# Optimization experiments

Hardware: AMD Instinct MI355X
Metric: run time of the kernel (lower is better)

Reference implementation:

```python
import jax, jax.numpy as jnp
import numpy as np

B, LQ, LK = 2, 4096, 512
Q_DIM, KV_DIM, D_ATTN, N_HEADS = 1024, 1024, 1024, 16
HDIM = D_ATTN // N_HEADS
LOOKBACK = 4
ROPE_MAX = 8192


def rope_tables(smax, hdim):
    inv_freq = 1.0 / (10000.0 ** (jnp.arange(0, hdim, 2, dtype=jnp.float32) / hdim))
    freqs = jnp.arange(smax, dtype=jnp.float32)[:, None] * inv_freq[None, :]  # [S, hdim/2]
    emb = jnp.concatenate([freqs, freqs], axis=-1)  # [S, hdim]
    return jnp.cos(emb), jnp.sin(emb)


def rotate_half(x):
    h = x.shape[-1] // 2
    return jnp.concatenate([-x[..., h:], x[..., :h]], axis=-1)


def setup_inputs() -> dict:
    key = jax.random.key(0)
    ks = jax.random.split(key, 8)
    q = jax.random.normal(ks[0], (B, LQ, Q_DIM), dtype=jnp.float32)
    kv = jax.random.normal(ks[1], (B, LK, KV_DIM), dtype=jnp.float32)
    q_pos_ids = jax.random.randint(ks[2], (B, LQ), 0, 4096)
    kv_pos_ids = jax.random.randint(ks[3], (LK,), 0, 4096)
    seg_id = jnp.sort(jax.random.randint(ks[4], (B, LQ), 0, LK), axis=-1)
    sc = 1.0 / np.sqrt(Q_DIM)
    Wq = jax.random.normal(ks[5], (Q_DIM, D_ATTN), dtype=jnp.float32) * sc
    Wkv = jax.random.normal(ks[6], (KV_DIM, 2 * D_ATTN), dtype=jnp.float32) * sc
    Wo = jax.random.normal(ks[7], (D_ATTN, Q_DIM), dtype=jnp.float32) * sc
    return {"q": q, "kv": kv, "q_pos_ids": q_pos_ids, "kv_pos_ids": kv_pos_ids,
            "seg_id": seg_id, "Wq": Wq, "Wkv": Wkv, "Wo": Wo}


def reference(q, kv, q_pos_ids, kv_pos_ids, seg_id, Wq, Wkv, Wo):
    Bq, Lq, _ = q.shape
    Lk = kv.shape[1]
    # projections + split heads -> [B, H, L, hdim]
    qh = (q @ Wq).reshape(Bq, Lq, N_HEADS, HDIM).transpose(0, 2, 1, 3)
    kvl = kv @ Wkv
    kh = kvl[..., :D_ATTN].reshape(Bq, Lk, N_HEADS, HDIM).transpose(0, 2, 1, 3)
    vh = kvl[..., D_ATTN:].reshape(Bq, Lk, N_HEADS, HDIM).transpose(0, 2, 1, 3)
    # gathered RoPE
    cos, sin = rope_tables(ROPE_MAX, HDIM)  # [S, hdim]
    qp = jnp.clip(q_pos_ids, 0, ROPE_MAX - 1)
    q_cos = cos[qp][:, None]  # [B,1,Lq,hdim]
    q_sin = sin[qp][:, None]
    qh = qh * q_cos + rotate_half(qh) * q_sin
    kp = jnp.clip(kv_pos_ids, 0, ROPE_MAX - 1)
    k_cos = cos[kp][None, None]  # [1,1,Lk,hdim]
    k_sin = sin[kp][None, None]
    kh = kh * k_cos + rotate_half(kh) * k_sin
    # segment lookback mask: keep iff seg_id - lookback <= k <= seg_id
    kidx = jnp.arange(Lk)
    keep = (kidx[None, None, :] <= seg_id[:, :, None]) & \
           (kidx[None, None, :] >= seg_id[:, :, None] - LOOKBACK)  # [B,Lq,Lk]
    scale = 1.0 / np.sqrt(HDIM)
    scores = jnp.einsum('bhqd,bhkd->bhqk', qh, kh) * scale
    scores = jnp.where(keep[:, None], scores, -jnp.inf)
    attn = jax.nn.softmax(scores, axis=-1)
    ctx = jnp.einsum('bhqk,bhkd->bhqd', attn, vh)
    out = ctx.transpose(0, 2, 1, 3).reshape(Bq, Lq, D_ATTN)
    return out @ Wo
```

## Files before the change

### kernel.cpp

```cpp
#include <hip/hip_runtime.h>
#include <math.h>


typedef unsigned short u16;
typedef __attribute__((ext_vector_type(8))) short bhalf8;
typedef __attribute__((ext_vector_type(4))) float fvec4;

__device__ __forceinline__ u16 f2bf(float f) {
  unsigned u = __float_as_uint(f);
  u += 0x7fffu + ((u >> 16) & 1u);
  return (u16)(u >> 16);
}
__device__ __forceinline__ float bf2f(u16 h) {
  return __uint_as_float(((unsigned)h) << 16);
}

__global__ __launch_bounds__(256) void prep_kernel(
    const float* __restrict__ Wq, const float* __restrict__ Wkv,
    const float* __restrict__ Wo, u16* __restrict__ WqT,
    u16* __restrict__ WkvT, u16* __restrict__ WoT,
    const float* __restrict__ q, u16* __restrict__ qb,
    const float* __restrict__ kv, u16* __restrict__ kvb,
    float2* __restrict__ csT) {
  const int bid = blockIdx.x;
  if (bid < 4096) {
    __shared__ float tile[32][33];
    const float* W;
    u16* Wt;
    int N, t;
    if (bid < 1024)      { W = Wq;  Wt = WqT;  N = 1024; t = bid; }
    else if (bid < 3072) { W = Wkv; Wt = WkvT; N = 2048; t = bid - 1024; }
    else                 { W = Wo;  Wt = WoT;  N = 1024; t = bid - 3072; }
    const int sh = (N >> 11) + 5;
    const int n0 = (t & ((1 << sh) - 1)) << 5;
    const int k0 = (t >> sh) << 5;
    const int tx = threadIdx.x & 31, ty = threadIdx.x >> 5;
#pragma unroll
    for (int i = 0; i < 32; i += 8)
      tile[ty + i][tx] = W[(size_t)(k0 + ty + i) * N + n0 + tx];
    __syncthreads();
#pragma unroll
    for (int i = 0; i < 32; i += 8)
      Wt[(size_t)(n0 + ty + i) * 1024 + k0 + tx] = f2bf(tile[tx][ty + i]);
    return;
  }
  const int NQ4 = 2097152, NKV4 = 262144, NR = 131072;
  const int stride = 2048 * 256;
  for (int u = (bid - 4096) * 256 + threadIdx.x; u < NQ4 + NKV4 + NR; u += stride) {
    if (u < NQ4) {
      const float4 v = ((const float4*)q)[u];
      ushort4 o;
      o.x = f2bf(v.x); o.y = f2bf(v.y); o.z = f2bf(v.z); o.w = f2bf(v.w);
      ((ushort4*)qb)[u] = o;
    } else if (u < NQ4 + NKV4) {
      const int i = u - NQ4;
      const float4 v = ((const float4*)kv)[i];
      ushort4 o;
      o.x = f2bf(v.x); o.y = f2bf(v.y); o.z = f2bf(v.z); o.w = f2bf(v.w);
      ((ushort4*)kvb)[i] = o;
    } else {
      const int i = u - NQ4 - NKV4;
      const int pos = i >> 5, j = i & 31;
      const float invf = expf(-(float)j * 0.28782313662425572f);
      float s, c;
      sincosf((float)pos * invf, &s, &c);
      csT[i] = make_float2(c, s);
    }
  }
}

__device__ __forceinline__ void gemm_core_128_db(
    const u16* __restrict__ A, const u16* __restrict__ Bt,
    int m0, int n0, fvec4 acc[4][4], u16* As, u16* Bs) {
  const int tid = threadIdx.x;
  const int lane = tid & 63;
  const int wv = tid >> 6, wm = wv >> 1, wn = wv & 1;

  int a_off[4], b_off[4];
#pragma unroll
  for (int i = 0; i < 4; ++i) {
    const int rA = wm * 64 + i * 16 + (lane & 15);
    a_off[i] = rA * 32 + (((lane >> 4) ^ ((rA >> 1) & 3)) << 3);
    const int rB = wn * 64 + i * 16 + (lane & 15);
    b_off[i] = rB * 32 + (((lane >> 4) ^ ((rB >> 1) & 3)) << 3);
  }
  const int i0 = tid, i1 = tid + 256;
  const int r0 = i0 >> 2, g0 = (i0 & 3) ^ ((r0 >> 1) & 3);
  const int r1 = i1 >> 2, g1 = (i1 & 3) ^ ((r1 >> 1) & 3);
  const u16* a0 = A + (size_t)(m0 + r0) * 1024 + g0 * 8;
  const u16* a1 = A + (size_t)(m0 + r1) * 1024 + g1 * 8;
  const u16* b0 = Bt + (size_t)(n0 + r0) * 1024 + g0 * 8;
  const u16* b1 = Bt + (size_t)(n0 + r1) * 1024 + g1 * 8;

#define STAGE_DB(buf, kk)                                                    \
  do {                                                                       \
    u16* As_ = As + (buf) * 4096;                                            \
    u16* Bs_ = Bs + (buf) * 4096;                                            \
    __builtin_amdgcn_global_load_lds(                                        \
        (__attribute__((address_space(1))) void*)(a0 + (kk)),                \
        (__attribute__((address_space(3))) void*)(As_ + i0 * 8), 16, 0, 0);  \
    __builtin_amdgcn_global_load_lds(                                        \
        (__attribute__((address_space(1))) void*)(a1 + (kk)),                \
        (__attribute__((address_space(3))) void*)(As_ + i1 * 8), 16, 0, 0);  \
    __builtin_amdgcn_global_load_lds(                                        \
        (__attribute__((address_space(1))) void*)(b0 + (kk)),                \
        (__attribute__((address_space(3))) void*)(Bs_ + i0 * 8), 16, 0, 0);  \
    __builtin_amdgcn_global_load_lds(                                        \
        (__attribute__((address_space(1))) void*)(b1 + (kk)),                \
        (__attribute__((address_space(3))) void*)(Bs_ + i1 * 8), 16, 0, 0);  \
  } while (0)

  STAGE_DB(0, 0);
  STAGE_DB(1, 32);
  asm volatile("s_waitcnt vmcnt(4)" ::: "memory");
  __builtin_amdgcn_s_barrier();

#pragma unroll
  for (int t = 0; t < 32; ++t) {
    const int cur = t % 3;
    const int nx2 = (t + 2) % 3;
    const int k2 = t * 32 + 64;
    if (k2 < 1024) STAGE_DB(nx2, k2);
    const int co = cur * 4096;
    bhalf8 af[4], bfv[4];
#pragma unroll
    for (int i = 0; i < 4; ++i) af[i] = *(const bhalf8*)(As + co + a_off[i]);
#pragma unroll
    for (int i = 0; i < 4; ++i) bfv[i] = *(const bhalf8*)(Bs + co + b_off[i]);
    __builtin_amdgcn_s_setprio(1);
#pragma unroll
    for (int mi = 0; mi < 4; ++mi)
#pragma unroll
      for (int ni = 0; ni < 4; ++ni)
        acc[mi][ni] = __builtin_amdgcn_mfma_f32_16x16x32_bf16(
            af[mi], bfv[ni], acc[mi][ni], 0, 0, 0);
    __builtin_amdgcn_s_setprio(0);
    if (k2 < 1024) {
      asm volatile("s_waitcnt vmcnt(4)" ::: "memory");
    } else {
      asm volatile("s_waitcnt vmcnt(0)" ::: "memory");
    }
    __builtin_amdgcn_s_barrier();
  }
#undef STAGE_DB
}

#define GEMM_PROLOGUE()                                              \
  __shared__ __align__(16) u16 As[3 * 128 * 32];                     \
  __shared__ __align__(16) u16 Bs[3 * 128 * 32];                     \
  fvec4 acc[4][4];                                                   \
  _Pragma("unroll") for (int i = 0; i < 4; ++i)                      \
      _Pragma("unroll") for (int j = 0; j < 4; ++j)                  \
          acc[i][j] = (fvec4){0.f, 0.f, 0.f, 0.f};

__global__ __launch_bounds__(256) void gemm12_kernel(
    const u16* __restrict__ qA, const u16* __restrict__ WqT,
    const u16* __restrict__ kvA, const u16* __restrict__ WkvT,
    u16* __restrict__ qh, u16* __restrict__ kh, u16* __restrict__ vh,
    const int* __restrict__ qpos, const int* __restrict__ kpos,
    const float2* __restrict__ csT) {
  GEMM_PROLOGUE();
  const int swz = ((blockIdx.x & 7) * 80) + (blockIdx.x >> 3);
  const int lane = threadIdx.x & 63;
  const int wv = threadIdx.x >> 6, wm = wv >> 1, wn = wv & 1;

  if (swz < 512) {
    const int m0 = (swz >> 3) * 128, n0 = (swz & 7) * 128;
    gemm_core_128_db(qA, WqT, m0, n0, acc, As, Bs);
#pragma unroll
    for (int mi = 0; mi < 4; ++mi) {
#pragma unroll
      for (int r = 0; r < 4; ++r) {
        const int rowg = m0 + wm * 64 + mi * 16 + (lane >> 4) * 4 + r;
        int pos = qpos[rowg];
        pos = pos < 0 ? 0 : (pos > 4095 ? 4095 : pos);
#pragma unroll
        for (int ni = 0; ni < 2; ++ni) {
          const int j = ni * 16 + (lane & 15);
          const float2 cs = csT[pos * 32 + j];
          const float x1 = acc[mi][ni][r], x2 = acc[mi][ni + 2][r];
          const int colg = n0 + wn * 64 + ni * 16 + (lane & 15);
          qh[(size_t)rowg * 1024 + colg]      = f2bf((x1 * cs.x - x2 * cs.y) * 0.125f);
          qh[(size_t)rowg * 1024 + colg + 32] = f2bf((x2 * cs.x + x1 * cs.y) * 0.125f);
        }
      }
    }
  } else {
    const int t = swz - 512;
    const int m0 = (t >> 4) * 128, n0 = (t & 15) * 128;
    gemm_core_128_db(kvA, WkvT, m0, n0, acc, As, Bs);
    const bool isK = (n0 + wn * 64) < 1024;
#pragma unroll
    for (int mi = 0; mi < 4; ++mi) {
#pragma unroll
      for (int r = 0; r < 4; ++r) {
        const int rowg = m0 + wm * 64 + mi * 16 + (lane >> 4) * 4 + r;
        if (isK) {
          int pos = kpos[rowg & 511];
          pos = pos < 0 ? 0 : (pos > 4095 ? 4095 : pos);
#pragma unroll
          for (int ni = 0; ni < 2; ++ni) {
            const int j = ni * 16 + (lane & 15);
            const float2 cs = csT[pos * 32 + j];
            const float x1 = acc[mi][ni][r], x2 = acc[mi][ni + 2][r];
            const int colg = n0 + wn * 64 + ni * 16 + (lane & 15);
            kh[(size_t)rowg * 1024 + colg]      = f2bf(x1 * cs.x - x2 * cs.y);
            kh[(size_t)rowg * 1024 + colg + 32] = f2bf(x2 * cs.x + x1 * cs.y);
          }
        } else {
#pragma unroll
          for (int ni = 0; ni < 4; ++ni) {
            const int colg = n0 + wn * 64 + ni * 16 + (lane & 15);
            vh[(size_t)rowg * 1024 + colg - 1024] = f2bf(acc[mi][ni][r]);
          }
        }
      }
    }
  }
}

__global__ __launch_bounds__(256) void gemm_out_kernel(
    const u16* __restrict__ A, const u16* __restrict__ Bt,
    float* __restrict__ out) {
  GEMM_PROLOGUE();
  const int wg = ((blockIdx.x & 7) << 6) + (blockIdx.x >> 3);
  const int m0 = (wg >> 3) * 128, n0 = (wg & 7) * 128;
  gemm_core_128_db(A, Bt, m0, n0, acc, As, Bs);
  const int lane = threadIdx.x & 63;
  const int wv = threadIdx.x >> 6, wm = wv >> 1, wn = wv & 1;
#pragma unroll
  for (int mi = 0; mi < 4; ++mi) {
#pragma unroll
    for (int r = 0; r < 4; ++r) {
      const int rowg = m0 + wm * 64 + mi * 16 + (lane >> 4) * 4 + r;
#pragma unroll
      for (int ni = 0; ni < 4; ++ni) {
        const int colg = n0 + wn * 64 + ni * 16 + (lane & 15);
        out[(size_t)rowg * 1024 + colg] = acc[mi][ni][r];
      }
    }
  }
}

__global__ __launch_bounds__(256) void attn_kernel(
    const u16* __restrict__ qh, const u16* __restrict__ kh,
    const u16* __restrict__ vh, const int* __restrict__ seg_id,
    u16* __restrict__ ctx) {
  const int lane = threadIdx.x & 63;
  const int row = (blockIdx.x * 256 + threadIdx.x) >> 6;
  const int b = row >> 12;
  const int sg = seg_id[row];
  const int kmin = sg > 4 ? sg - 4 : 0;

  const u16* qp = qh + (size_t)row * 1024 + lane * 16;
  const bhalf8 qa = *(const bhalf8*)qp;
  const bhalf8 qb = *(const bhalf8*)(qp + 8);
  float qv[16];
#pragma unroll
  for (int e = 0; e < 8; ++e) {
    qv[e] = bf2f((u16)qa[e]);
    qv[8 + e] = bf2f((u16)qb[e]);
  }

  float sc[5];
  float mx = -3.0e38f;
#pragma unroll
  for (int t = 0; t < 5; ++t) {
    const int k = kmin + t;
    const u16* kp = kh + (size_t)((b << 9) + k) * 1024 + lane * 16;
    const bhalf8 ka = *(const bhalf8*)kp;
    const bhalf8 kb = *(const bhalf8*)(kp + 8);
    float d = 0.f;
#pragma unroll
    for (int e = 0; e < 8; ++e)
      d += qv[e] * bf2f((u16)ka[e]) + qv[8 + e] * bf2f((u16)kb[e]);
    d += __shfl_xor(d, 1);
    d += __shfl_xor(d, 2);
    sc[t] = (k <= sg) ? d : -3.0e38f;
    mx = fmaxf(mx, sc[t]);
  }

  float den = 0.f;
  float o[16];
#pragma unroll
  for (int e = 0; e < 16; ++e) o[e] = 0.f;
#pragma unroll
  for (int t = 0; t < 5; ++t) {
    const float p = __expf(sc[t] - mx);
    den += p;
    const int k = kmin + t;
    const u16* vp = vh + (size_t)((b << 9) + k) * 1024 + lane * 16;
    const bhalf8 va = *(const bhalf8*)vp;
    const bhalf8 vb = *(const bhalf8*)(vp + 8);
#pragma unroll
    for (int e = 0; e < 8; ++e) {
      o[e] += p * bf2f((u16)va[e]);
      o[8 + e] += p * bf2f((u16)vb[e]);
    }
  }
  const float inv = 1.f / den;
  bhalf8 oa, ob;
#pragma unroll
  for (int e = 0; e < 8; ++e) {
    oa[e] = (short)f2bf(o[e] * inv);
    ob[e] = (short)f2bf(o[8 + e] * inv);
  }
  u16* cp = ctx + (size_t)row * 1024 + lane * 16;
  *(bhalf8*)cp = oa;
  *(bhalf8*)(cp + 8) = ob;
}

extern "C" void kernel_launch(void* const* d_in, const int* in_sizes, int n_in,
                              void* d_out, int out_size, void* d_ws, size_t ws_size,
                              hipStream_t stream) {
  const float* q   = (const float*)d_in[0];
  const float* kv  = (const float*)d_in[1];
  const int* qpos  = (const int*)d_in[2];
  const int* kpos  = (const int*)d_in[3];
  const int* seg   = (const int*)d_in[4];
  const float* Wq  = (const float*)d_in[5];
  const float* Wkv = (const float*)d_in[6];
  const float* Wo  = (const float*)d_in[7];
  float* out = (float*)d_out;

  char* w = (char*)d_ws;
  u16* qb    = (u16*)w; w += (size_t)8192 * 1024 * 2;
  u16* kvb   = (u16*)w; w += (size_t)1024 * 1024 * 2;
  u16* WqT   = (u16*)w; w += (size_t)1024 * 1024 * 2;
  u16* WkvT  = (u16*)w; w += (size_t)2048 * 1024 * 2;
  u16* WoT   = (u16*)w; w += (size_t)1024 * 1024 * 2;
  u16* qhB   = (u16*)w; w += (size_t)8192 * 1024 * 2;
  u16* khB   = (u16*)w; w += (size_t)1024 * 1024 * 2;
  u16* vhB   = (u16*)w; w += (size_t)1024 * 1024 * 2;
  u16* ctxB  = (u16*)w; w += (size_t)8192 * 1024 * 2;
  float2* csT = (float2*)w; w += (size_t)4096 * 32 * 8;

  prep_kernel<<<6144, 256, 0, stream>>>(Wq, Wkv, Wo, WqT, WkvT, WoT,
                                        q, qb, kv, kvb, csT);
  gemm12_kernel<<<640, 256, 0, stream>>>(qb, WqT, kvb, WkvT,
                                         qhB, khB, vhB, qpos, kpos, csT);
  attn_kernel<<<2048, 256, 0, stream>>>(qhB, khB, vhB, seg, ctxB);
  gemm_out_kernel<<<512, 256, 0, stream>>>(ctxB, WoT, out);
}
```

Measured before the change: 92.44 us.

## Split GEMM workgroups into producer and consumer waves for LDS staging

GEMM kernels now launch 512 threads: four waves issue global-to-LDS loads into a triple buffer, and four waves only read LDS and run MFMAs, synchronized by raw s_barrier. This is meant to keep the MFMA waves free of load issue and vmcnt waits. The trade-off is doubled workgroup size, which may reduce occupancy given the accumulator register footprint, plus idle producer waves during the epilogue.

```diff
diff --git a/kernel.cpp b/kernel.cpp
--- a/kernel.cpp
+++ b/kernel.cpp
@@ -69,30 +69,23 @@
   }
 }
 
-__device__ __forceinline__ void gemm_core_128_db(
+__device__ __forceinline__ void gemm_core_128_pc(
     const u16* __restrict__ A, const u16* __restrict__ Bt,
     int m0, int n0, fvec4 acc[4][4], u16* As, u16* Bs) {
   const int tid = threadIdx.x;
-  const int lane = tid & 63;
-  const int wv = tid >> 6, wm = wv >> 1, wn = wv & 1;
-
-  int a_off[4], b_off[4];
-#pragma unroll
-  for (int i = 0; i < 4; ++i) {
-    const int rA = wm * 64 + i * 16 + (lane & 15);
-    a_off[i] = rA * 32 + (((lane >> 4) ^ ((rA >> 1) & 3)) << 3);
-    const int rB = wn * 64 + i * 16 + (lane & 15);
-    b_off[i] = rB * 32 + (((lane >> 4) ^ ((rB >> 1) & 3)) << 3);
-  }
-  const int i0 = tid, i1 = tid + 256;
-  const int r0 = i0 >> 2, g0 = (i0 & 3) ^ ((r0 >> 1) & 3);
-  const int r1 = i1 >> 2, g1 = (i1 & 3) ^ ((r1 >> 1) & 3);
-  const u16* a0 = A + (size_t)(m0 + r0) * 1024 + g0 * 8;
-  const u16* a1 = A + (size_t)(m0 + r1) * 1024 + g1 * 8;
-  const u16* b0 = Bt + (size_t)(n0 + r0) * 1024 + g0 * 8;
-  const u16* b1 = Bt + (size_t)(n0 + r1) * 1024 + g1 * 8;
-
-#define STAGE_DB(buf, kk)                                                    \
+  const int wv = tid >> 6;
+
+  if (wv >= 4) {
+    const int t2 = tid & 255;
+    const int i0 = t2, i1 = t2 + 256;
+    const int r0 = i0 >> 2, g0 = (i0 & 3) ^ ((r0 >> 1) & 3);
+    const int r1 = i1 >> 2, g1 = (i1 & 3) ^ ((r1 >> 1) & 3);
+    const u16* a0 = A + (size_t)(m0 + r0) * 1024 + g0 * 8;
+    const u16* a1 = A + (size_t)(m0 + r1) * 1024 + g1 * 8;
+    const u16* b0 = Bt + (size_t)(n0 + r0) * 1024 + g0 * 8;
+    const u16* b1 = Bt + (size_t)(n0 + r1) * 1024 + g1 * 8;
+
+#define STAGE_PC(buf, kk)                                                    \
   do {                                                                       \
     u16* As_ = As + (buf) * 4096;                                            \
     u16* Bs_ = Bs + (buf) * 4096;                                            \
@@ -110,39 +103,52 @@
         (__attribute__((address_space(3))) void*)(Bs_ + i1 * 8), 16, 0, 0);  \
   } while (0)
 
-  STAGE_DB(0, 0);
-  STAGE_DB(1, 32);
-  asm volatile("s_waitcnt vmcnt(4)" ::: "memory");
-  __builtin_amdgcn_s_barrier();
-
-#pragma unroll
-  for (int t = 0; t < 32; ++t) {
-    const int cur = t % 3;
-    const int nx2 = (t + 2) % 3;
-    const int k2 = t * 32 + 64;
-    if (k2 < 1024) STAGE_DB(nx2, k2);
-    const int co = cur * 4096;
-    bhalf8 af[4], bfv[4];
-#pragma unroll
-    for (int i = 0; i < 4; ++i) af[i] = *(const bhalf8*)(As + co + a_off[i]);
-#pragma unroll
-    for (int i = 0; i < 4; ++i) bfv[i] = *(const bhalf8*)(Bs + co + b_off[i]);
-    __builtin_amdgcn_s_setprio(1);
-#pragma unroll
-    for (int mi = 0; mi < 4; ++mi)
-#pragma unroll
-      for (int ni = 0; ni < 4; ++ni)
-        acc[mi][ni] = __builtin_amdgcn_mfma_f32_16x16x32_bf16(
-            af[mi], bfv[ni], acc[mi][ni], 0, 0, 0);
-    __builtin_amdgcn_s_setprio(0);
-    if (k2 < 1024) {
-      asm volatile("s_waitcnt vmcnt(4)" ::: "memory");
-    } else {
-      asm volatile("s_waitcnt vmcnt(0)" ::: "memory");
-    }
-    __builtin_amdgcn_s_barrier();
-  }
-#undef STAGE_DB
+    STAGE_PC(0, 0);
+    STAGE_PC(1, 32);
+    asm volatile("s_waitcnt vmcnt(4)" ::: "memory");
+    asm volatile("s_barrier" ::: "memory");
+#pragma unroll
+    for (int t = 0; t < 32; ++t) {
+      if (t < 30) {
+        STAGE_PC((t + 2) % 3, (t + 2) * 32);
+        asm volatile("s_waitcnt vmcnt(4)" ::: "memory");
+      } else {
+        asm volatile("s_waitcnt vmcnt(0)" ::: "memory");
+      }
+      asm volatile("s_barrier" ::: "memory");
+    }
+#undef STAGE_PC
+  } else {
+    const int lane = tid & 63;
+    const int wm = wv >> 1, wn = wv & 1;
+    int a_off[4], b_off[4];
+#pragma unroll
+    for (int i = 0; i < 4; ++i) {
+      const int rA = wm * 64 + i * 16 + (lane & 15);
+      a_off[i] = rA * 32 + (((lane >> 4) ^ ((rA >> 1) & 3)) << 3);
+      const int rB = wn * 64 + i * 16 + (lane & 15);
+      b_off[i] = rB * 32 + (((lane >> 4) ^ ((rB >> 1) & 3)) << 3);
+    }
+    asm volatile("s_barrier" ::: "memory");
+#pragma unroll
+    for (int t = 0; t < 32; ++t) {
+      const int co = (t % 3) * 4096;
+      bhalf8 af[4], bfv[4];
+#pragma unroll
+      for (int i = 0; i < 4; ++i) af[i] = *(const bhalf8*)(As + co + a_off[i]);
+#pragma unroll
+      for (int i = 0; i < 4; ++i) bfv[i] = *(const bhalf8*)(Bs + co + b_off[i]);
+      __builtin_amdgcn_s_setprio(1);
+#pragma unroll
+      for (int mi = 0; mi < 4; ++mi)
+#pragma unroll
+        for (int ni = 0; ni < 4; ++ni)
+          acc[mi][ni] = __builtin_amdgcn_mfma_f32_16x16x32_bf16(
+              af[mi], bfv[ni], acc[mi][ni], 0, 0, 0);
+      __builtin_amdgcn_s_setprio(0);
+      asm volatile("s_barrier" ::: "memory");
+    }
+  }
 }
 
 #define GEMM_PROLOGUE()                                              \
@@ -153,7 +159,7 @@
       _Pragma("unroll") for (int j = 0; j < 4; ++j)                  \
           acc[i][j] = (fvec4){0.f, 0.f, 0.f, 0.f};
 
-__global__ __launch_bounds__(256) void gemm12_kernel(
+__global__ __launch_bounds__(512) void gemm12_kernel(
     const u16* __restrict__ qA, const u16* __restrict__ WqT,
     const u16* __restrict__ kvA, const u16* __restrict__ WkvT,
     u16* __restrict__ qh, u16* __restrict__ kh, u16* __restrict__ vh,
@@ -162,11 +168,23 @@
   GEMM_PROLOGUE();
   const int swz = ((blockIdx.x & 7) * 80) + (blockIdx.x >> 3);
   const int lane = threadIdx.x & 63;
-  const int wv = threadIdx.x >> 6, wm = wv >> 1, wn = wv & 1;
-
+  const int wv = threadIdx.x >> 6;
+  const int wm = (wv & 3) >> 1, wn = wv & 1;
+
+  const u16 *A, *Bt;
+  int m0, n0;
   if (swz < 512) {
-    const int m0 = (swz >> 3) * 128, n0 = (swz & 7) * 128;
-    gemm_core_128_db(qA, WqT, m0, n0, acc, As, Bs);
+    A = qA; Bt = WqT;
+    m0 = (swz >> 3) * 128; n0 = (swz & 7) * 128;
+  } else {
+    const int t = swz - 512;
+    A = kvA; Bt = WkvT;
+    m0 = (t >> 4) * 128; n0 = (t & 15) * 128;
+  }
+  gemm_core_128_pc(A, Bt, m0, n0, acc, As, Bs);
+  if (wv >= 4) return;
+
+  if (swz < 512) {
 #pragma unroll
     for (int mi = 0; mi < 4; ++mi) {
 #pragma unroll
@@ -186,9 +204,6 @@
       }
     }
   } else {
-    const int t = swz - 512;
-    const int m0 = (t >> 4) * 128, n0 = (t & 15) * 128;
-    gemm_core_128_db(kvA, WkvT, m0, n0, acc, As, Bs);
     const bool isK = (n0 + wn * 64) < 1024;
 #pragma unroll
     for (int mi = 0; mi < 4; ++mi) {
@@ -219,15 +234,17 @@
   }
 }
 
-__global__ __launch_bounds__(256) void gemm_out_kernel(
+__global__ __launch_bounds__(512) void gemm_out_kernel(
     const u16* __restrict__ A, const u16* __restrict__ Bt,
     float* __restrict__ out) {
   GEMM_PROLOGUE();
   const int wg = ((blockIdx.x & 7) << 6) + (blockIdx.x >> 3);
   const int m0 = (wg >> 3) * 128, n0 = (wg & 7) * 128;
-  gemm_core_128_db(A, Bt, m0, n0, acc, As, Bs);
+  gemm_core_128_pc(A, Bt, m0, n0, acc, As, Bs);
+  const int wv = threadIdx.x >> 6;
+  if (wv >= 4) return;
   const int lane = threadIdx.x & 63;
-  const int wv = threadIdx.x >> 6, wm = wv >> 1, wn = wv & 1;
+  const int wm = wv >> 1, wn = wv & 1;
 #pragma unroll
   for (int mi = 0; mi < 4; ++mi) {
 #pragma unroll
@@ -337,8 +354,8 @@
 
   prep_kernel<<<6144, 256, 0, stream>>>(Wq, Wkv, Wo, WqT, WkvT, WoT,
                                         q, qb, kv, kvb, csT);
-  gemm12_kernel<<<640, 256, 0, stream>>>(qb, WqT, kvb, WkvT,
+  gemm12_kernel<<<640, 512, 0, stream>>>(qb, WqT, kvb, WkvT,
                                          qhB, khB, vhB, qpos, kpos, csT);
   attn_kernel<<<2048, 256, 0, stream>>>(qhB, khB, vhB, seg, ctxB);
-  gemm_out_kernel<<<512, 256, 0, stream>>>(ctxB, WoT, out);
-}
+  gemm_out_kernel<<<512, 512, 0, stream>>>(ctxB, WoT, out);
+}
```

After: 93.00 us. No clear change (+0.6%).

## Switch GEMMs to 256x128 tiles with 512 threads and 8-phase pipelined K loop

Applied to the files above, without the earlier changes.

The GEMM core moves from 128x128 tiles with K-step 32 and 256 threads to 256x128 tiles with K-step 64 and 8 waves. The K loop is split into eight phases that interleave staged global-to-LDS loads with MFMA sub-blocks, using barriers between phases and a new XOR swizzle over 8 chunks. The aim is more reuse per loaded byte and better overlap of loads with MFMA. In exchange it uses much more LDS per block, launches half as many blocks (320 and 256), and adds barrier overhead.

```diff
diff --git a/kernel.cpp b/kernel.cpp
--- a/kernel.cpp
+++ b/kernel.cpp
@@ -5,6 +5,8 @@
 typedef unsigned short u16;
 typedef __attribute__((ext_vector_type(8))) short bhalf8;
 typedef __attribute__((ext_vector_type(4))) float fvec4;
+
+#define MFMA(a, b, c) __builtin_amdgcn_mfma_f32_16x16x32_bf16((a), (b), (c), 0, 0, 0)
 
 __device__ __forceinline__ u16 f2bf(float f) {
   unsigned u = __float_as_uint(f);
@@ -69,104 +71,150 @@
   }
 }
 
-__device__ __forceinline__ void gemm_core_128_db(
+__device__ __forceinline__ void gemm_core_8ph(
     const u16* __restrict__ A, const u16* __restrict__ Bt,
     int m0, int n0, fvec4 acc[4][4], u16* As, u16* Bs) {
   const int tid = threadIdx.x;
   const int lane = tid & 63;
   const int wv = tid >> 6, wm = wv >> 1, wn = wv & 1;
 
-  int a_off[4], b_off[4];
-#pragma unroll
-  for (int i = 0; i < 4; ++i) {
-    const int rA = wm * 64 + i * 16 + (lane & 15);
-    a_off[i] = rA * 32 + (((lane >> 4) ^ ((rA >> 1) & 3)) << 3);
-    const int rB = wn * 64 + i * 16 + (lane & 15);
-    b_off[i] = rB * 32 + (((lane >> 4) ^ ((rB >> 1) & 3)) << 3);
-  }
-  const int i0 = tid, i1 = tid + 256;
-  const int r0 = i0 >> 2, g0 = (i0 & 3) ^ ((r0 >> 1) & 3);
-  const int r1 = i1 >> 2, g1 = (i1 & 3) ^ ((r1 >> 1) & 3);
-  const u16* a0 = A + (size_t)(m0 + r0) * 1024 + g0 * 8;
-  const u16* a1 = A + (size_t)(m0 + r1) * 1024 + g1 * 8;
-  const u16* b0 = Bt + (size_t)(n0 + r0) * 1024 + g0 * 8;
-  const u16* b1 = Bt + (size_t)(n0 + r1) * 1024 + g1 * 8;
-
-#define STAGE_DB(buf, kk)                                                    \
+  const u16* aglb[4];
+  int aldst[4];
+#pragma unroll
+  for (int j = 0; j < 4; ++j) {
+    const int cidx = tid + j * 512;
+    const int row = cidx >> 3, g = (cidx & 7) ^ (row & 7);
+    aglb[j] = A + (size_t)(m0 + row) * 1024 + g * 8;
+    aldst[j] = cidx * 8;
+  }
+  const u16* bglb[2];
+  int bldst[2];
+#pragma unroll
+  for (int j = 0; j < 2; ++j) {
+    const int cidx = tid + j * 512;
+    const int row = cidx >> 3, g = (cidx & 7) ^ (row & 7);
+    bglb[j] = Bt + (size_t)(n0 + row) * 1024 + g * 8;
+    bldst[j] = cidx * 8;
+  }
+
+#define LD_A(buf, kk, j)                                                     \
+  __builtin_amdgcn_global_load_lds(                                          \
+      (__attribute__((address_space(1))) void*)(aglb[j] + (kk)),             \
+      (__attribute__((address_space(3))) void*)(As + (buf) * 16384 + aldst[j]), 16, 0, 0)
+#define LD_B(buf, kk, j)                                                     \
+  __builtin_amdgcn_global_load_lds(                                          \
+      (__attribute__((address_space(1))) void*)(bglb[j] + (kk)),             \
+      (__attribute__((address_space(3))) void*)(Bs + (buf) * 8192 + bldst[j]), 16, 0, 0)
+
+  const int c = lane >> 4;
+  const int sl0 = ((c) ^ (lane & 7)) * 8;
+  const int sl1 = ((c + 4) ^ (lane & 7)) * 8;
+  const int rba = (wm * 64 + (lane & 15)) * 64;
+  const int rbb = (wn * 64 + (lane & 15)) * 64;
+
+#define PH(bufi, QM, QN, STAGE, TAIL)                                        \
   do {                                                                       \
-    u16* As_ = As + (buf) * 4096;                                            \
-    u16* Bs_ = Bs + (buf) * 4096;                                            \
-    __builtin_amdgcn_global_load_lds(                                        \
-        (__attribute__((address_space(1))) void*)(a0 + (kk)),                \
-        (__attribute__((address_space(3))) void*)(As_ + i0 * 8), 16, 0, 0);  \
-    __builtin_amdgcn_global_load_lds(                                        \
-        (__attribute__((address_space(1))) void*)(a1 + (kk)),                \
-        (__attribute__((address_space(3))) void*)(As_ + i1 * 8), 16, 0, 0);  \
-    __builtin_amdgcn_global_load_lds(                                        \
-        (__attribute__((address_space(1))) void*)(b0 + (kk)),                \
-        (__attribute__((address_space(3))) void*)(Bs_ + i0 * 8), 16, 0, 0);  \
-    __builtin_amdgcn_global_load_lds(                                        \
-        (__attribute__((address_space(1))) void*)(b1 + (kk)),                \
-        (__attribute__((address_space(3))) void*)(Bs_ + i1 * 8), 16, 0, 0);  \
+    STAGE;                                                                   \
+    const u16* Ab = As + (bufi) * 16384 + rba;                               \
+    const u16* Bb = Bs + (bufi) * 8192 + rbb;                                \
+    const bhalf8 a00 = *(const bhalf8*)(Ab + (QM * 2) * 1024 + sl0);         \
+    const bhalf8 a01 = *(const bhalf8*)(Ab + (QM * 2) * 1024 + sl1);         \
+    const bhalf8 a10 = *(const bhalf8*)(Ab + (QM * 2 + 1) * 1024 + sl0);     \
+    const bhalf8 a11 = *(const bhalf8*)(Ab + (QM * 2 + 1) * 1024 + sl1);     \
+    const bhalf8 b00 = *(const bhalf8*)(Bb + (QN * 2) * 1024 + sl0);         \
+    const bhalf8 b01 = *(const bhalf8*)(Bb + (QN * 2) * 1024 + sl1);         \
+    const bhalf8 b10 = *(const bhalf8*)(Bb + (QN * 2 + 1) * 1024 + sl0);     \
+    const bhalf8 b11 = *(const bhalf8*)(Bb + (QN * 2 + 1) * 1024 + sl1);     \
+    __builtin_amdgcn_s_barrier();                                            \
+    __builtin_amdgcn_s_setprio(1);                                           \
+    acc[QM * 2][QN * 2]         = MFMA(a00, b00, acc[QM * 2][QN * 2]);       \
+    acc[QM * 2][QN * 2]         = MFMA(a01, b01, acc[QM * 2][QN * 2]);       \
+    acc[QM * 2][QN * 2 + 1]     = MFMA(a00, b10, acc[QM * 2][QN * 2 + 1]);   \
+    acc[QM * 2][QN * 2 + 1]     = MFMA(a01, b11, acc[QM * 2][QN * 2 + 1]);   \
+    acc[QM * 2 + 1][QN * 2]     = MFMA(a10, b00, acc[QM * 2 + 1][QN * 2]);   \
+    acc[QM * 2 + 1][QN * 2]     = MFMA(a11, b01, acc[QM * 2 + 1][QN * 2]);   \
+    acc[QM * 2 + 1][QN * 2 + 1] = MFMA(a10, b10, acc[QM * 2 + 1][QN * 2 + 1]);\
+    acc[QM * 2 + 1][QN * 2 + 1] = MFMA(a11, b11, acc[QM * 2 + 1][QN * 2 + 1]);\
+    __builtin_amdgcn_s_setprio(0);                                           \
+    TAIL;                                                                    \
   } while (0)
 
-  STAGE_DB(0, 0);
-  STAGE_DB(1, 32);
-  asm volatile("s_waitcnt vmcnt(4)" ::: "memory");
+#define BAR __builtin_amdgcn_s_barrier()
+#define VMTAIL(st)                                                           \
+  do {                                                                       \
+    if (st) asm volatile("s_waitcnt vmcnt(6)" ::: "memory");                 \
+    else    asm volatile("s_waitcnt vmcnt(0)" ::: "memory");                 \
+    __builtin_amdgcn_s_barrier();                                            \
+  } while (0)
+
+#pragma unroll
+  for (int j = 0; j < 4; ++j) LD_A(0, 0, j);
+#pragma unroll
+  for (int j = 0; j < 2; ++j) LD_B(0, 0, j);
+#pragma unroll
+  for (int j = 0; j < 4; ++j) LD_A(1, 64, j);
+#pragma unroll
+  for (int j = 0; j < 2; ++j) LD_B(1, 64, j);
+  asm volatile("s_waitcnt vmcnt(6)" ::: "memory");
   __builtin_amdgcn_s_barrier();
 
-#pragma unroll
-  for (int t = 0; t < 32; ++t) {
-    const int cur = t % 3;
-    const int nx2 = (t + 2) % 3;
-    const int k2 = t * 32 + 64;
-    if (k2 < 1024) STAGE_DB(nx2, k2);
-    const int co = cur * 4096;
-    bhalf8 af[4], bfv[4];
-#pragma unroll
-    for (int i = 0; i < 4; ++i) af[i] = *(const bhalf8*)(As + co + a_off[i]);
-#pragma unroll
-    for (int i = 0; i < 4; ++i) bfv[i] = *(const bhalf8*)(Bs + co + b_off[i]);
-    __builtin_amdgcn_s_setprio(1);
-#pragma unroll
-    for (int mi = 0; mi < 4; ++mi)
-#pragma unroll
-      for (int ni = 0; ni < 4; ++ni)
-        acc[mi][ni] = __builtin_amdgcn_mfma_f32_16x16x32_bf16(
-            af[mi], bfv[ni], acc[mi][ni], 0, 0, 0);
-    __builtin_amdgcn_s_setprio(0);
-    if (k2 < 1024) {
-      asm volatile("s_waitcnt vmcnt(4)" ::: "memory");
-    } else {
-      asm volatile("s_waitcnt vmcnt(0)" ::: "memory");
-    }
-    __builtin_amdgcn_s_barrier();
-  }
-#undef STAGE_DB
+  int b0 = 0;
+#pragma unroll 1
+  for (int it = 0; it < 8; ++it) {
+    const int b1 = (b0 == 2) ? 0 : b0 + 1;
+    const int b2 = (b1 == 2) ? 0 : b1 + 1;
+    const int kk2 = it * 128 + 128;
+    const int kk3 = it * 128 + 192;
+    const bool st = it < 7;
+    PH(b0, 0, 0, if (st) { LD_A(b2, kk2, 0); LD_A(b2, kk2, 1); }, BAR);
+    PH(b0, 0, 1, if (st) { LD_A(b2, kk2, 2); LD_A(b2, kk2, 3); }, BAR);
+    PH(b0, 1, 0, if (st) { LD_B(b2, kk2, 0); LD_B(b2, kk2, 1); }, BAR);
+    PH(b0, 1, 1, (void)0, VMTAIL(st));
+    PH(b1, 0, 0, if (st) { LD_A(b0, kk3, 0); LD_A(b0, kk3, 1); }, BAR);
+    PH(b1, 0, 1, if (st) { LD_A(b0, kk3, 2); LD_A(b0, kk3, 3); }, BAR);
+    PH(b1, 1, 0, if (st) { LD_B(b0, kk3, 0); LD_B(b0, kk3, 1); }, BAR);
+    PH(b1, 1, 1, (void)0, VMTAIL(st));
+    b0 = b2;
+  }
+#undef PH
+#undef BAR
+#undef VMTAIL
+#undef LD_A
+#undef LD_B
 }
 
 #define GEMM_PROLOGUE()                                              \
-  __shared__ __align__(16) u16 As[3 * 128 * 32];                     \
-  __shared__ __align__(16) u16 Bs[3 * 128 * 32];                     \
+  __shared__ __align__(16) u16 As[3 * 256 * 64];                     \
+  __shared__ __align__(16) u16 Bs[3 * 128 * 64];                     \
   fvec4 acc[4][4];                                                   \
   _Pragma("unroll") for (int i = 0; i < 4; ++i)                      \
       _Pragma("unroll") for (int j = 0; j < 4; ++j)                  \
           acc[i][j] = (fvec4){0.f, 0.f, 0.f, 0.f};
 
-__global__ __launch_bounds__(256) void gemm12_kernel(
+__global__ __launch_bounds__(512) void gemm12_kernel(
     const u16* __restrict__ qA, const u16* __restrict__ WqT,
     const u16* __restrict__ kvA, const u16* __restrict__ WkvT,
     u16* __restrict__ qh, u16* __restrict__ kh, u16* __restrict__ vh,
     const int* __restrict__ qpos, const int* __restrict__ kpos,
     const float2* __restrict__ csT) {
   GEMM_PROLOGUE();
-  const int swz = ((blockIdx.x & 7) * 80) + (blockIdx.x >> 3);
+  const int swz = ((blockIdx.x & 7) * 40) + (blockIdx.x >> 3);
   const int lane = threadIdx.x & 63;
   const int wv = threadIdx.x >> 6, wm = wv >> 1, wn = wv & 1;
 
-  if (swz < 512) {
-    const int m0 = (swz >> 3) * 128, n0 = (swz & 7) * 128;
-    gemm_core_128_db(qA, WqT, m0, n0, acc, As, Bs);
+  const u16 *A, *Bt;
+  int m0, n0;
+  if (swz < 256) {
+    A = qA; Bt = WqT;
+    m0 = (swz >> 3) * 256; n0 = (swz & 7) * 128;
+  } else {
+    const int t = swz - 256;
+    A = kvA; Bt = WkvT;
+    m0 = (t >> 4) * 256; n0 = (t & 15) * 128;
+  }
+  gemm_core_8ph(A, Bt, m0, n0, acc, As, Bs);
+
+  if (swz < 256) {
 #pragma unroll
     for (int mi = 0; mi < 4; ++mi) {
 #pragma unroll
@@ -186,9 +234,6 @@
       }
     }
   } else {
-    const int t = swz - 512;
-    const int m0 = (t >> 4) * 128, n0 = (t & 15) * 128;
-    gemm_core_128_db(kvA, WkvT, m0, n0, acc, As, Bs);
     const bool isK = (n0 + wn * 64) < 1024;
 #pragma unroll
     for (int mi = 0; mi < 4; ++mi) {
@@ -219,13 +264,13 @@
   }
 }
 
-__global__ __launch_bounds__(256) void gemm_out_kernel(
+__global__ __launch_bounds__(512) void gemm_out_kernel(
     const u16* __restrict__ A, const u16* __restrict__ Bt,
     float* __restrict__ out) {
   GEMM_PROLOGUE();
-  const int wg = ((blockIdx.x & 7) << 6) + (blockIdx.x >> 3);
-  const int m0 = (wg >> 3) * 128, n0 = (wg & 7) * 128;
-  gemm_core_128_db(A, Bt, m0, n0, acc, As, Bs);
+  const int wg = ((blockIdx.x & 7) << 5) + (blockIdx.x >> 3);
+  const int m0 = (wg >> 3) * 256, n0 = (wg & 7) * 128;
+  gemm_core_8ph(A, Bt, m0, n0, acc, As, Bs);
   const int lane = threadIdx.x & 63;
   const int wv = threadIdx.x >> 6, wm = wv >> 1, wn = wv & 1;
 #pragma unroll
@@ -337,8 +382,8 @@
 
   prep_kernel<<<6144, 256, 0, stream>>>(Wq, Wkv, Wo, WqT, WkvT, WoT,
                                         q, qb, kv, kvb, csT);
-  gemm12_kernel<<<640, 256, 0, stream>>>(qb, WqT, kvb, WkvT,
+  gemm12_kernel<<<320, 512, 0, stream>>>(qb, WqT, kvb, WkvT,
                                          qhB, khB, vhB, qpos, kpos, csT);
   attn_kernel<<<2048, 256, 0, stream>>>(qhB, khB, vhB, seg, ctxB);
-  gemm_out_kernel<<<512, 256, 0, stream>>>(ctxB, WoT, out);
-}
+  gemm_out_kernel<<<256, 512, 0, stream>>>(ctxB, WoT, out);
+}
```

Result: slower. 145.1 us (+57.0%).

## Split 128x128 GEMM tiles across eight waves and interleave Q/KV blocks

Applied to the files above, without the earlier changes.

The two GEMM kernels now launch 512 threads per block, so eight waves share each 128x128 tile. Each wave computes a 32x64 sub-tile with half the accumulators, and each thread issues one A and one B global-to-LDS load per stage instead of two of each. The gemm12 block mapping also interleaves KV-projection blocks among Q-projection blocks (one in five) so the two kinds are spread across the grid. The aim is more waves in flight to hide latency, with lower register use per wave, at the cost of more LDS fragment reads per MFMA and barriers spanning more waves.

```diff
diff --git a/kernel.cpp b/kernel.cpp
--- a/kernel.cpp
+++ b/kernel.cpp
@@ -5,6 +5,8 @@
 typedef unsigned short u16;
 typedef __attribute__((ext_vector_type(8))) short bhalf8;
 typedef __attribute__((ext_vector_type(4))) float fvec4;
+
+#define MFMA(a, b, c) __builtin_amdgcn_mfma_f32_16x16x32_bf16((a), (b), (c), 0, 0, 0)
 
 __device__ __forceinline__ u16 f2bf(float f) {
   unsigned u = __float_as_uint(f);
@@ -69,91 +71,82 @@
   }
 }
 
-__device__ __forceinline__ void gemm_core_128_db(
+__device__ __forceinline__ void gemm_core_8w(
     const u16* __restrict__ A, const u16* __restrict__ Bt,
-    int m0, int n0, fvec4 acc[4][4], u16* As, u16* Bs) {
+    int m0, int n0, fvec4 acc[2][4], u16* As, u16* Bs) {
   const int tid = threadIdx.x;
   const int lane = tid & 63;
   const int wv = tid >> 6, wm = wv >> 1, wn = wv & 1;
 
-  int a_off[4], b_off[4];
+  int a_off[2], b_off[4];
+#pragma unroll
+  for (int i = 0; i < 2; ++i) {
+    const int rA = wm * 32 + i * 16 + (lane & 15);
+    a_off[i] = rA * 32 + (((lane >> 4) ^ ((rA >> 1) & 3)) << 3);
+  }
 #pragma unroll
   for (int i = 0; i < 4; ++i) {
-    const int rA = wm * 64 + i * 16 + (lane & 15);
-    a_off[i] = rA * 32 + (((lane >> 4) ^ ((rA >> 1) & 3)) << 3);
     const int rB = wn * 64 + i * 16 + (lane & 15);
     b_off[i] = rB * 32 + (((lane >> 4) ^ ((rB >> 1) & 3)) << 3);
   }
-  const int i0 = tid, i1 = tid + 256;
-  const int r0 = i0 >> 2, g0 = (i0 & 3) ^ ((r0 >> 1) & 3);
-  const int r1 = i1 >> 2, g1 = (i1 & 3) ^ ((r1 >> 1) & 3);
-  const u16* a0 = A + (size_t)(m0 + r0) * 1024 + g0 * 8;
-  const u16* a1 = A + (size_t)(m0 + r1) * 1024 + g1 * 8;
-  const u16* b0 = Bt + (size_t)(n0 + r0) * 1024 + g0 * 8;
-  const u16* b1 = Bt + (size_t)(n0 + r1) * 1024 + g1 * 8;
-
-#define STAGE_DB(buf, kk)                                                    \
+  const int rS = tid >> 2, gS = (tid & 3) ^ ((rS >> 1) & 3);
+  const u16* ag = A + (size_t)(m0 + rS) * 1024 + gS * 8;
+  const u16* bg = Bt + (size_t)(n0 + rS) * 1024 + gS * 8;
+  const int ldst = tid * 8;
+
+#define STAGE2(buf, kk)                                                      \
   do {                                                                       \
-    u16* As_ = As + (buf) * 4096;                                            \
-    u16* Bs_ = Bs + (buf) * 4096;                                            \
     __builtin_amdgcn_global_load_lds(                                        \
-        (__attribute__((address_space(1))) void*)(a0 + (kk)),                \
-        (__attribute__((address_space(3))) void*)(As_ + i0 * 8), 16, 0, 0);  \
+        (__attribute__((address_space(1))) void*)(ag + (kk)),                \
+        (__attribute__((address_space(3))) void*)(As + (buf) * 4096 + ldst), \
+        16, 0, 0);                                                           \
     __builtin_amdgcn_global_load_lds(                                        \
-        (__attribute__((address_space(1))) void*)(a1 + (kk)),                \
-        (__attribute__((address_space(3))) void*)(As_ + i1 * 8), 16, 0, 0);  \
-    __builtin_amdgcn_global_load_lds(                                        \
-        (__attribute__((address_space(1))) void*)(b0 + (kk)),                \
-        (__attribute__((address_space(3))) void*)(Bs_ + i0 * 8), 16, 0, 0);  \
-    __builtin_amdgcn_global_load_lds(                                        \
-        (__attribute__((address_space(1))) void*)(b1 + (kk)),                \
-        (__attribute__((address_space(3))) void*)(Bs_ + i1 * 8), 16, 0, 0);  \
+        (__attribute__((address_space(1))) void*)(bg + (kk)),                \
+        (__attribute__((address_space(3))) void*)(Bs + (buf) * 4096 + ldst), \
+        16, 0, 0);                                                           \
   } while (0)
 
-  STAGE_DB(0, 0);
-  STAGE_DB(1, 32);
-  asm volatile("s_waitcnt vmcnt(4)" ::: "memory");
+  STAGE2(0, 0);
+  STAGE2(1, 32);
+  asm volatile("s_waitcnt vmcnt(2)" ::: "memory");
   __builtin_amdgcn_s_barrier();
 
 #pragma unroll
   for (int t = 0; t < 32; ++t) {
-    const int cur = t % 3;
-    const int nx2 = (t + 2) % 3;
     const int k2 = t * 32 + 64;
-    if (k2 < 1024) STAGE_DB(nx2, k2);
-    const int co = cur * 4096;
-    bhalf8 af[4], bfv[4];
-#pragma unroll
-    for (int i = 0; i < 4; ++i) af[i] = *(const bhalf8*)(As + co + a_off[i]);
+    if (k2 < 1024) STAGE2((t + 2) % 3, k2);
+    const int co = (t % 3) * 4096;
+    bhalf8 af[2], bfv[4];
+#pragma unroll
+    for (int i = 0; i < 2; ++i) af[i] = *(const bhalf8*)(As + co + a_off[i]);
 #pragma unroll
     for (int i = 0; i < 4; ++i) bfv[i] = *(const bhalf8*)(Bs + co + b_off[i]);
     __builtin_amdgcn_s_setprio(1);
 #pragma unroll
-    for (int mi = 0; mi < 4; ++mi)
+    for (int mi = 0; mi < 2; ++mi)
 #pragma unroll
       for (int ni = 0; ni < 4; ++ni)
-        acc[mi][ni] = __builtin_amdgcn_mfma_f32_16x16x32_bf16(
-            af[mi], bfv[ni], acc[mi][ni], 0, 0, 0);
+        acc[mi][ni] = MFMA(af[mi], bfv[ni], acc[mi][ni]);
     __builtin_amdgcn_s_setprio(0);
     if (k2 < 1024) {
-      asm volatile("s_waitcnt vmcnt(4)" ::: "memory");
+      asm volatile("s_waitcnt vmcnt(2)" ::: "memory");
     } else {
       asm volatile("s_waitcnt vmcnt(0)" ::: "memory");
     }
     __builtin_amdgcn_s_barrier();
   }
-#undef STAGE_DB
+#undef STAGE2
 }
 
 #define GEMM_PROLOGUE()                                              \
   __shared__ __align__(16) u16 As[3 * 128 * 32];                     \
   __shared__ __align__(16) u16 Bs[3 * 128 * 32];                     \
-  fvec4 acc[4][4];                                                   \
-  _Pragma("unroll") for (int i = 0; i < 4; ++i)                      \
+  fvec4 acc[2][4];                                                   \
+  _Pragma("unroll") for (int i = 0; i < 2; ++i)                      \
       _Pragma("unroll") for (int j = 0; j < 4; ++j)                  \
           acc[i][j] = (fvec4){0.f, 0.f, 0.f, 0.f};
 
-__global__ __launch_bounds__(256) void gemm12_kernel(
+__global__ __launch_bounds__(512) void gemm12_kernel(
     const u16* __restrict__ qA, const u16* __restrict__ WqT,
     const u16* __restrict__ kvA, const u16* __restrict__ WkvT,
     u16* __restrict__ qh, u16* __restrict__ kh, u16* __restrict__ vh,
@@ -161,17 +154,30 @@
     const float2* __restrict__ csT) {
   GEMM_PROLOGUE();
   const int swz = ((blockIdx.x & 7) * 80) + (blockIdx.x >> 3);
+  const int q5 = swz / 5, r5 = swz - q5 * 5;
+  const bool isQ = (r5 < 4);
   const int lane = threadIdx.x & 63;
   const int wv = threadIdx.x >> 6, wm = wv >> 1, wn = wv & 1;
 
-  if (swz < 512) {
-    const int m0 = (swz >> 3) * 128, n0 = (swz & 7) * 128;
-    gemm_core_128_db(qA, WqT, m0, n0, acc, As, Bs);
-#pragma unroll
-    for (int mi = 0; mi < 4; ++mi) {
+  const u16 *A, *Bt;
+  int m0, n0;
+  if (isQ) {
+    const int id = q5 * 4 + r5;
+    A = qA; Bt = WqT;
+    m0 = (id >> 3) * 128; n0 = (id & 7) * 128;
+  } else {
+    const int id = q5;
+    A = kvA; Bt = WkvT;
+    m0 = (id >> 4) * 128; n0 = (id & 15) * 128;
+  }
+  gemm_core_8w(A, Bt, m0, n0, acc, As, Bs);
+
+  if (isQ) {
+#pragma unroll
+    for (int mi = 0; mi < 2; ++mi) {
 #pragma unroll
       for (int r = 0; r < 4; ++r) {
-        const int rowg = m0 + wm * 64 + mi * 16 + (lane >> 4) * 4 + r;
+        const int rowg = m0 + wm * 32 + mi * 16 + (lane >> 4) * 4 + r;
         int pos = qpos[rowg];
         pos = pos < 0 ? 0 : (pos > 4095 ? 4095 : pos);
 #pragma unroll
@@ -186,15 +192,12 @@
       }
     }
   } else {
-    const int t = swz - 512;
-    const int m0 = (t >> 4) * 128, n0 = (t & 15) * 128;
-    gemm_core_128_db(kvA, WkvT, m0, n0, acc, As, Bs);
     const bool isK = (n0 + wn * 64) < 1024;
 #pragma unroll
-    for (int mi = 0; mi < 4; ++mi) {
+    for (int mi = 0; mi < 2; ++mi) {
 #pragma unroll
       for (int r = 0; r < 4; ++r) {
-        const int rowg = m0 + wm * 64 + mi * 16 + (lane >> 4) * 4 + r;
+        const int rowg = m0 + wm * 32 + mi * 16 + (lane >> 4) * 4 + r;
         if (isK) {
           int pos = kpos[rowg & 511];
           pos = pos < 0 ? 0 : (pos > 4095 ? 4095 : pos);
@@ -219,20 +222,20 @@
   }
 }
 
-__global__ __launch_bounds__(256) void gemm_out_kernel(
+__global__ __launch_bounds__(512) void gemm_out_kernel(
     const u16* __restrict__ A, const u16* __restrict__ Bt,
     float* __restrict__ out) {
   GEMM_PROLOGUE();
   const int wg = ((blockIdx.x & 7) << 6) + (blockIdx.x >> 3);
   const int m0 = (wg >> 3) * 128, n0 = (wg & 7) * 128;
-  gemm_core_128_db(A, Bt, m0, n0, acc, As, Bs);
+  gemm_core_8w(A, Bt, m0, n0, acc, As, Bs);
   const int lane = threadIdx.x & 63;
   const int wv = threadIdx.x >> 6, wm = wv >> 1, wn = wv & 1;
 #pragma unroll
-  for (int mi = 0; mi < 4; ++mi) {
+  for (int mi = 0; mi < 2; ++mi) {
 #pragma unroll
     for (int r = 0; r < 4; ++r) {
-      const int rowg = m0 + wm * 64 + mi * 16 + (lane >> 4) * 4 + r;
+      const int rowg = m0 + wm * 32 + mi * 16 + (lane >> 4) * 4 + r;
 #pragma unroll
       for (int ni = 0; ni < 4; ++ni) {
         const int colg = n0 + wn * 64 + ni * 16 + (lane & 15);
@@ -337,8 +340,8 @@
 
   prep_kernel<<<6144, 256, 0, stream>>>(Wq, Wkv, Wo, WqT, WkvT, WoT,
                                         q, qb, kv, kvb, csT);
-  gemm12_kernel<<<640, 256, 0, stream>>>(qb, WqT, kvb, WkvT,
+  gemm12_kernel<<<640, 512, 0, stream>>>(qb, WqT, kvb, WkvT,
                                          qhB, khB, vhB, qpos, kpos, csT);
   attn_kernel<<<2048, 256, 0, stream>>>(qhB, khB, vhB, seg, ctxB);
-  gemm_out_kernel<<<512, 256, 0, stream>>>(ctxB, WoT, out);
-}
+  gemm_out_kernel<<<512, 512, 0, stream>>>(ctxB, WoT, out);
+}
```

Measured after the change: 93.10 us. Within noise of the previous version (+0.7%).
